# Kernel optimization log

Measured on AMD Instinct MI355X. Metric: run time of the kernel, lower is better.

The kernel has to match this reference:

```python
import jax, jax.numpy as jnp
import numpy as np

NX = 256
NY = 256
H = 1.0          # grid spacing (h == h_sub since scale_sub == 1)
N_ITERS = 512    # parallel (Jacobi) Godunov sweeps; wavefront moves ~1 cell/iter
BIG = 1.0e6      # 'infinity' init for travel times
N_PICKS = 2_000_000


def setup_inputs() -> dict:
    key = jax.random.key(0)
    k1, k2, k3, k4, k5 = jax.random.split(key, 5)
    # slowness f = 1/vp with vp ~ U[5,6] km/s (realistic crustal P velocities)
    vp = 5.0 + jax.random.uniform(k1, (NX, NY), dtype=jnp.float32)
    f = 1.0 / vp
    # station (source) location in grid units, strictly inside the grid
    src_xy = jax.random.uniform(k2, (2,), dtype=jnp.float32) * jnp.array(
        [NX - 1.0, NY - 1.0], dtype=jnp.float32)
    # event locations in grid units and origin times
    event_x = jax.random.uniform(k3, (N_PICKS,), dtype=jnp.float32) * (NX - 1.0)
    event_y = jax.random.uniform(k4, (N_PICKS,), dtype=jnp.float32) * (NY - 1.0)
    event_time = jax.random.normal(k5, (N_PICKS,), dtype=jnp.float32)
    return {"f": f, "src_xy": src_xy, "event_x": event_x,
            "event_y": event_y, "event_time": event_time}


def _st_clamp(x, lo, hi):
    # straight-through clamp (matches torch Clamp.backward: identity grad)
    return x + jax.lax.stop_gradient(jnp.clip(x, lo, hi) - x)


def _eikonal2d(f, src_xy):
    """Godunov upwind eikonal solve |grad u| = f on an NX x NY grid,
    point source at fractional coords src_xy, via fixed-point Jacobi sweeps."""
    sx, sy = src_xy[0], src_xy[1]
    ix0 = jnp.clip(jnp.floor(sx), 0, NX - 2).astype(jnp.int32)
    iy0 = jnp.clip(jnp.floor(sy), 0, NY - 2).astype(jnp.int32)
    # seed the 4 cells around the source with local straight-ray times
    ii = jnp.stack([ix0, ix0, ix0 + 1, ix0 + 1])
    jj = jnp.stack([iy0, iy0 + 1, iy0, iy0 + 1])
    d = jnp.sqrt((ii.astype(f.dtype) - sx) ** 2 +
                 (jj.astype(f.dtype) - sy) ** 2) * H * f[ii, jj]
    u0 = jnp.full((NX, NY), BIG, dtype=f.dtype).at[ii, jj].set(d)
    fh = f * H

    def step(u, _):
        up = jnp.pad(u, 1, constant_values=BIG)
        a = jnp.minimum(up[:-2, 1:-1], up[2:, 1:-1])   # upwind min along x
        b = jnp.minimum(up[1:-1, :-2], up[1:-1, 2:])   # upwind min along y
        one_sided = jnp.minimum(a, b) + fh
        disc = jnp.maximum(2.0 * fh * fh - (a - b) ** 2, 0.0)
        two_sided = 0.5 * (a + b + jnp.sqrt(disc))
        cand = jnp.where(jnp.abs(a - b) >= fh, one_sided, two_sided)
        return jnp.minimum(u, cand), None

    u, _ = jax.lax.scan(step, u0, None, length=N_ITERS)
    return u


def _interp(tt, x, y):
    # bilinear interp exactly as Eikonal2D.interp (floor+clamp, 4 gathers)
    nx, ny = tt.shape
    ix0 = jnp.clip(jnp.floor(x), 0, nx - 2).astype(jnp.int32)
    iy0 = jnp.clip(jnp.floor(y), 0, ny - 2).astype(jnp.int32)
    ix1 = ix0 + 1
    iy1 = iy0 + 1
    xc = _st_clamp(x, 0.0, nx - 1.0)
    yc = _st_clamp(y, 0.0, ny - 1.0)
    Q00 = tt[ix0, iy0]
    Q01 = tt[ix0, iy1]
    Q10 = tt[ix1, iy0]
    Q11 = tt[ix1, iy1]
    return (Q00 * (ix1 - xc) * (iy1 - yc) + Q10 * (xc - ix0) * (iy1 - yc)
            + Q01 * (ix1 - xc) * (yc - iy0) + Q11 * (xc - ix0) * (yc - iy0))


def reference(f, src_xy, event_x, event_y, event_time):
    u = _eikonal2d(f, src_xy)                 # [NX, NY] travel-time table
    tt = _interp(u, event_x, event_y)         # [N] per-pick travel times
    return event_time + tt                    # predicted arrival times [N]
```

## Files before the change

kernel.cpp:

```cpp
#include <hip/hip_runtime.h>
#include <math.h>

#define NXg 256
#define NYg 256
#define BIGV 1.0e6f
#define TB 32
#define KMAX 96
#define NSWEEP 24

__global__ void eik_init(const float* __restrict__ f, const float* __restrict__ src,
                         float* __restrict__ u) {
    int t = blockIdx.x * blockDim.x + threadIdx.x;
    float sx = src[0], sy = src[1];
    int ix0 = (int)fminf(fmaxf(floorf(sx), 0.f), (float)(NXg - 2));
    int iy0 = (int)fminf(fmaxf(floorf(sy), 0.f), (float)(NYg - 2));
#pragma unroll
    for (int k = 0; k < 4; ++k) {
        int cid = t + (k << 14);
        int gx = cid >> 8, gy = cid & 255;
        float val = BIGV;
        if ((gx == ix0 || gx == ix0 + 1) && (gy == iy0 || gy == iy0 + 1)) {
            float dx = (float)gx - sx, dy = (float)gy - sy;
            val = sqrtf(dx * dx + dy * dy) * f[cid];
        }
        u[cid] = val;
    }
}

__global__ __launch_bounds__(256) void eik_sweep(const float* __restrict__ f,
                                                 float* __restrict__ u) {
    __shared__ float us[TB + 2][TB + 2];
    const int t = threadIdx.x;
    const int bx = blockIdx.x & 7, by = blockIdx.x >> 3;
    const int x0 = bx * TB, y0 = by * TB;

    for (int idx = t; idx < (TB + 2) * (TB + 2); idx += 256) {
        int r = idx / (TB + 2), c = idx % (TB + 2);
        int gx = x0 + r - 1, gy = y0 + c - 1;
        float v = BIGV;
        if (gx >= 0 && gx < NXg && gy >= 0 && gy < NYg) v = u[(gx << 8) + gy];
        us[r][c] = v;
    }

    float fhr[4], tfh2[4];
#pragma unroll
    for (int k = 0; k < 4; ++k) {
        int cid = t + (k << 8);
        int r = cid >> 5, c = cid & 31;
        float fv = f[((x0 + r) << 8) + (y0 + c)];
        fhr[k] = fv;
        tfh2[k] = 2.0f * fv * fv;
    }
    __syncthreads();

    for (int it = 0; it < KMAX; ++it) {
        int ch = 0;
#pragma unroll
        for (int k = 0; k < 4; ++k) {
            int cid = t + (k << 8);
            int r = cid >> 5, c = cid & 31;
            float a  = fminf(us[r][c + 1], us[r + 2][c + 1]);
            float b  = fminf(us[r + 1][c], us[r + 1][c + 2]);
            float u0 = us[r + 1][c + 1];
            float one  = fminf(a, b) + fhr[k];
            float diff = a - b;
            float disc = fmaxf(tfh2[k] - diff * diff, 0.f);
            float two  = 0.5f * (a + b + sqrtf(disc));
            float cand = (fabsf(diff) >= fhr[k]) ? one : two;
            if (cand < u0) { us[r + 1][c + 1] = cand; ch = 1; }
        }
        if (__syncthreads_count(ch) == 0) break;
    }

#pragma unroll
    for (int k = 0; k < 4; ++k) {
        int cid = t + (k << 8);
        int r = cid >> 5, c = cid & 31;
        u[((x0 + r) << 8) + (y0 + c)] = us[r + 1][c + 1];
    }
}

__global__ void eik_interp(const float* __restrict__ u,
                           const float* __restrict__ ex,
                           const float* __restrict__ ey,
                           const float* __restrict__ et,
                           float* __restrict__ out, int n) {
    int i = blockIdx.x * blockDim.x + threadIdx.x;
    int stride = gridDim.x * blockDim.x;
    for (; i < n; i += stride) {
        float x = ex[i], y = ey[i];
        int ix0 = (int)fminf(fmaxf(floorf(x), 0.f), (float)(NXg - 2));
        int iy0 = (int)fminf(fmaxf(floorf(y), 0.f), (float)(NYg - 2));
        float xc = fminf(fmaxf(x, 0.f), (float)(NXg - 1));
        float yc = fminf(fmaxf(y, 0.f), (float)(NYg - 1));
        float fx0 = (float)ix0, fy0 = (float)iy0;
        float wx0 = xc - fx0, wx1 = (fx0 + 1.f) - xc;
        float wy0 = yc - fy0, wy1 = (fy0 + 1.f) - yc;
        int base = (ix0 << 8) + iy0;
        float Q00 = u[base],       Q01 = u[base + 1];
        float Q10 = u[base + 256], Q11 = u[base + 257];
        float tt = Q00 * wx1 * wy1 + Q10 * wx0 * wy1
                 + Q01 * wx1 * wy0 + Q11 * wx0 * wy0;
        out[i] = et[i] + tt;
    }
}

extern "C" void kernel_launch(void* const* d_in, const int* in_sizes, int n_in,
                              void* d_out, int out_size, void* d_ws, size_t ws_size,
                              hipStream_t stream) {
    const float* f   = (const float*)d_in[0];
    const float* src = (const float*)d_in[1];
    const float* ex  = (const float*)d_in[2];
    const float* ey  = (const float*)d_in[3];
    const float* et  = (const float*)d_in[4];
    float* out = (float*)d_out;
    float* u   = (float*)d_ws;
    int n = in_sizes[2];

    eik_init<<<64, 256, 0, stream>>>(f, src, u);
    for (int r = 0; r < NSWEEP; ++r)
        eik_sweep<<<64, 256, 0, stream>>>(f, u);
    eik_interp<<<2048, 256, 0, stream>>>(u, ex, ey, et, out, n);
}
```

Baseline: 910.6 us.

## Replace block Jacobi sweeps with wavefront fast-sweeping on 64x64 tiles

Replaces the 32x32-tile Jacobi relaxation with a Gauss-Seidel fast-sweeping scheme on 64x64 tiles. Each wave of 64 threads sweeps the tile along anti-diagonals in one of four directions, using volatile shared memory, and updates values in place. Tiles that hold no finite values exit early. The launch count drops from 24 to 8 rounds of 16 blocks. This should need far fewer iterations to converge, but four waves write the same tile concurrently without synchronisation between diagonal steps, and only 16 blocks occupy the GPU.

```diff
diff --git a/kernel.cpp b/kernel.cpp
--- a/kernel.cpp
+++ b/kernel.cpp
@@ -4,9 +4,10 @@
 #define NXg 256
 #define NYg 256
 #define BIGV 1.0e6f
-#define TB 32
-#define KMAX 96
-#define NSWEEP 24
+#define UP 66
+#define FP 66
+#define NROUNDS 8
+#define MAXSETS 6
 
 __global__ void eik_init(const float* __restrict__ f, const float* __restrict__ src,
                          float* __restrict__ u) {
@@ -27,56 +28,82 @@
     }
 }
 
-__global__ __launch_bounds__(256) void eik_sweep(const float* __restrict__ f,
-                                                 float* __restrict__ u) {
-    __shared__ float us[TB + 2][TB + 2];
+__device__ __forceinline__ float eik_relax(float u0, float a, float b, float fh) {
+    float one  = fminf(a, b) + fh;
+    float diff = a - b;
+    float disc = fmaxf(2.0f * fh * fh - diff * diff, 0.0f);
+    float two  = 0.5f * (a + b + sqrtf(disc));
+    float cand = (fabsf(diff) >= fh) ? one : two;
+    return fminf(u0, cand);
+}
+
+__global__ __launch_bounds__(256) void eik_fsm(const float* __restrict__ f,
+                                               float* __restrict__ u) {
+    __shared__ float uLs[66 * UP];
+    __shared__ float fL[64 * FP];
+    __shared__ int   sflag[4];
+    __shared__ int   s_seen;
+    volatile float* uL = uLs;
+
     const int t = threadIdx.x;
-    const int bx = blockIdx.x & 7, by = blockIdx.x >> 3;
-    const int x0 = bx * TB, y0 = by * TB;
+    const int l = t & 63;
+    const int w = t >> 6;
+    const int bx = blockIdx.x & 3, by = blockIdx.x >> 2;
+    const int x0 = bx * 64, y0 = by * 64;
 
-    for (int idx = t; idx < (TB + 2) * (TB + 2); idx += 256) {
-        int r = idx / (TB + 2), c = idx % (TB + 2);
+    if (t < 4) sflag[t] = 0;
+    if (t == 0) s_seen = 0;
+    __syncthreads();
+
+    int seen = 0;
+    for (int idx = t; idx < 66 * 66; idx += 256) {
+        int r = idx / 66, c = idx % 66;
         int gx = x0 + r - 1, gy = y0 + c - 1;
         float v = BIGV;
         if (gx >= 0 && gx < NXg && gy >= 0 && gy < NYg) v = u[(gx << 8) + gy];
-        us[r][c] = v;
+        uLs[r * UP + c] = v;
+        seen |= (v < BIGV) ? 1 : 0;
+    }
+    for (int idx = t; idx < 64 * 64; idx += 256) {
+        int r = idx >> 6, c = idx & 63;
+        fL[r * FP + c] = f[((x0 + r) << 8) + (y0 + c)];
+    }
+    if (seen) s_seen = 1;
+    __syncthreads();
+    if (!s_seen) return;
+
+    for (int set = 0; set < MAXSETS; ++set) {
+        int changed = 0;
+        for (int tt = 0; tt < 127; ++tt) {
+            int j = (w == 0) ? (tt - l)
+                  : (w == 1) ? (tt - 63 + l)
+                  : (w == 2) ? (63 - tt + l)
+                             : (126 - tt - l);
+            if (j >= 0 && j <= 63) {
+                float u0 = uL[(l + 1) * UP + (j + 1)];
+                float xm = uL[ l      * UP + (j + 1)];
+                float xp = uL[(l + 2) * UP + (j + 1)];
+                float ym = uL[(l + 1) * UP +  j     ];
+                float yp = uL[(l + 1) * UP + (j + 2)];
+                float fh = fL[l * FP + j];
+                float un = eik_relax(u0, fminf(xm, xp), fminf(ym, yp), fh);
+                if (un < u0) { uL[(l + 1) * UP + (j + 1)] = un; changed = 1; }
+            }
+        }
+        int anyc = __any(changed) ? 1 : 0;
+        __syncthreads();
+        if (l == 0) sflag[w] = anyc;
+        __syncthreads();
+        int tot = sflag[0] | sflag[1] | sflag[2] | sflag[3];
+        __syncthreads();
+        if (t < 4) sflag[t] = 0;
+        if (!tot) break;
     }
 
-    float fhr[4], tfh2[4];
-#pragma unroll
-    for (int k = 0; k < 4; ++k) {
-        int cid = t + (k << 8);
-        int r = cid >> 5, c = cid & 31;
-        float fv = f[((x0 + r) << 8) + (y0 + c)];
-        fhr[k] = fv;
-        tfh2[k] = 2.0f * fv * fv;
-    }
     __syncthreads();
-
-    for (int it = 0; it < KMAX; ++it) {
-        int ch = 0;
-#pragma unroll
-        for (int k = 0; k < 4; ++k) {
-            int cid = t + (k << 8);
-            int r = cid >> 5, c = cid & 31;
-            float a  = fminf(us[r][c + 1], us[r + 2][c + 1]);
-            float b  = fminf(us[r + 1][c], us[r + 1][c + 2]);
-            float u0 = us[r + 1][c + 1];
-            float one  = fminf(a, b) + fhr[k];
-            float diff = a - b;
-            float disc = fmaxf(tfh2[k] - diff * diff, 0.f);
-            float two  = 0.5f * (a + b + sqrtf(disc));
-            float cand = (fabsf(diff) >= fhr[k]) ? one : two;
-            if (cand < u0) { us[r + 1][c + 1] = cand; ch = 1; }
-        }
-        if (__syncthreads_count(ch) == 0) break;
-    }
-
-#pragma unroll
-    for (int k = 0; k < 4; ++k) {
-        int cid = t + (k << 8);
-        int r = cid >> 5, c = cid & 31;
-        u[((x0 + r) << 8) + (y0 + c)] = us[r + 1][c + 1];
+    for (int idx = t; idx < 64 * 64; idx += 256) {
+        int r = idx >> 6, c = idx & 63;
+        u[((x0 + r) << 8) + (y0 + c)] = uLs[(r + 1) * UP + (c + 1)];
     }
 }
 
@@ -118,7 +145,7 @@
     int n = in_sizes[2];
 
     eik_init<<<64, 256, 0, stream>>>(f, src, u);
-    for (int r = 0; r < NSWEEP; ++r)
-        eik_sweep<<<64, 256, 0, stream>>>(f, u);
+    for (int r = 0; r < NROUNDS; ++r)
+        eik_fsm<<<16, 256, 0, stream>>>(f, u);
     eik_interp<<<2048, 256, 0, stream>>>(u, ex, ey, et, out, n);
 }
```

Result: slower. 1.831 ms (+101.0%).

## Solve eikonal in one block with fast-sweeping wavefronts over fp16 shared grid

Applied to the files above, without the earlier changes.

Replaces the 24 launches of tiled Jacobi sweeps with a single-block solver. The whole 256x256 travel-time grid is held in LDS as fp16 values rounded upward. Each of the four wavefronts runs a Gauss-Seidel fast sweep from a different corner as an anti-diagonal wavefront across lanes, passing neighbour values by shuffles and repeating until nothing changes. The aim is to cut the launch count and the many Jacobi iterations, but everything now runs on one CU and the fp16 storage loses precision in the travel times.

```diff
diff --git a/kernel.cpp b/kernel.cpp
--- a/kernel.cpp
+++ b/kernel.cpp
@@ -1,83 +1,115 @@
 #include <hip/hip_runtime.h>
+#include <hip/hip_fp16.h>
 #include <math.h>
 
-#define NXg 256
-#define NYg 256
-#define BIGV 1.0e6f
-#define TB 32
-#define KMAX 96
-#define NSWEEP 24
+#define BIGF   57344.0f
+#define BIG2   0x7B007B00u
+#define MAXSETS 8
 
-__global__ void eik_init(const float* __restrict__ f, const float* __restrict__ src,
-                         float* __restrict__ u) {
-    int t = blockIdx.x * blockDim.x + threadIdx.x;
-    float sx = src[0], sy = src[1];
-    int ix0 = (int)fminf(fmaxf(floorf(sx), 0.f), (float)(NXg - 2));
-    int iy0 = (int)fminf(fmaxf(floorf(sy), 0.f), (float)(NYg - 2));
-#pragma unroll
-    for (int k = 0; k < 4; ++k) {
-        int cid = t + (k << 14);
-        int gx = cid >> 8, gy = cid & 255;
-        float val = BIGV;
-        if ((gx == ix0 || gx == ix0 + 1) && (gy == iy0 || gy == iy0 + 1)) {
-            float dx = (float)gx - sx, dy = (float)gy - sy;
-            val = sqrtf(dx * dx + dy * dy) * f[cid];
-        }
-        u[cid] = val;
-    }
+
+__device__ __forceinline__ float relax1(float u0, float a, float b, float fh) {
+    float one  = fminf(a, b) + fh;
+    float diff = a - b;
+    float disc = fmaxf(2.0f * fh * fh - diff * diff, 0.0f);
+    float two  = 0.5f * (a + b + sqrtf(disc));
+    float cand = (fabsf(diff) >= fh) ? one : two;
+    return fminf(u0, cand);
 }
 
-__global__ __launch_bounds__(256) void eik_sweep(const float* __restrict__ f,
-                                                 float* __restrict__ u) {
-    __shared__ float us[TB + 2][TB + 2];
-    const int t = threadIdx.x;
-    const int bx = blockIdx.x & 7, by = blockIdx.x >> 3;
-    const int x0 = bx * TB, y0 = by * TB;
+__device__ __forceinline__ unsigned short f2h_up(float x) {
+    __half h = __float2half(x);
+    if (__half2float(h) < x)
+        h = __ushort_as_half((unsigned short)(__half_as_ushort(h) + 1));
+    return __half_as_ushort(h);
+}
 
-    for (int idx = t; idx < (TB + 2) * (TB + 2); idx += 256) {
-        int r = idx / (TB + 2), c = idx % (TB + 2);
-        int gx = x0 + r - 1, gy = y0 + c - 1;
-        float v = BIGV;
-        if (gx >= 0 && gx < NXg && gy >= 0 && gy < NYg) v = u[(gx << 8) + gy];
-        us[r][c] = v;
+__global__ __launch_bounds__(256) void eik_solve(const float* __restrict__ f,
+                                                 const float* __restrict__ src,
+                                                 float* __restrict__ u_out) {
+    __shared__ unsigned short uW[65536];
+    const int t = threadIdx.x, l = t & 63, w = t >> 6;
+
+    {
+        unsigned int* p = (unsigned int*)uW;
+        for (int i = t; i < 32768; i += 256) p[i] = BIG2;
     }
-
-    float fhr[4], tfh2[4];
-#pragma unroll
-    for (int k = 0; k < 4; ++k) {
-        int cid = t + (k << 8);
-        int r = cid >> 5, c = cid & 31;
-        float fv = f[((x0 + r) << 8) + (y0 + c)];
-        fhr[k] = fv;
-        tfh2[k] = 2.0f * fv * fv;
+    __syncthreads();
+    if (t < 4) {
+        float sx = src[0], sy = src[1];
+        int ix0 = (int)fminf(fmaxf(floorf(sx), 0.f), 254.f);
+        int iy0 = (int)fminf(fmaxf(floorf(sy), 0.f), 254.f);
+        int gx = ix0 + (t >> 1), gy = iy0 + (t & 1);
+        float dx = (float)gx - sx, dy = (float)gy - sy;
+        float v = sqrtf(dx * dx + dy * dy) * f[(gx << 8) + gy];
+        uW[(gx << 8) + gy] = f2h_up(v);
     }
     __syncthreads();
 
-    for (int it = 0; it < KMAX; ++it) {
-        int ch = 0;
-#pragma unroll
-        for (int k = 0; k < 4; ++k) {
-            int cid = t + (k << 8);
-            int r = cid >> 5, c = cid & 31;
-            float a  = fminf(us[r][c + 1], us[r + 2][c + 1]);
-            float b  = fminf(us[r + 1][c], us[r + 1][c + 2]);
-            float u0 = us[r + 1][c + 1];
-            float one  = fminf(a, b) + fhr[k];
-            float diff = a - b;
-            float disc = fmaxf(tfh2[k] - diff * diff, 0.f);
-            float two  = 0.5f * (a + b + sqrtf(disc));
-            float cand = (fabsf(diff) >= fhr[k]) ? one : two;
-            if (cand < u0) { us[r + 1][c + 1] = cand; ch = 1; }
-        }
-        if (__syncthreads_count(ch) == 0) break;
+    const int xflip = w & 1, yflip = (w >> 1) & 1;
+    const int C0 = l << 2;
+    const int xk0 = xflip ? 255 - C0 : C0;
+    const int dxk = xflip ? -1 : 1;
+    const int ub0 = (xk0) << 8,            ub1 = (xk0 + dxk) << 8;
+    const int ub2 = (xk0 + 2 * dxk) << 8,  ub3 = (xk0 + 3 * dxk) << 8;
+    const float* fB0 = f + ub0; const float* fB1 = f + ub1;
+    const float* fB2 = f + ub2; const float* fB3 = f + ub3;
+
+#define YPHYS(S, K) ({ int yl_ = (S) - C0 - (K);                                \
+                       int yc_ = min(max(yl_, 0), 255);                         \
+                       yflip ? 255 - yc_ : yc_; })
+
+#define KSTEP(K, XM, YM, UN) {                                                  \
+        const int Y  = Yb - (K);                                                \
+        const int ycp = yflip ? 255 - min(max(Y, 0), 255)                       \
+                              : min(max(Y, 0), 255);                            \
+        const int off = ub##K + ycp;                                            \
+        unsigned short ob = uW[off];                                            \
+        float u0 = __half2float(__ushort_as_half(ob));                          \
+        float nu = relax1(u0, (XM), (YM), fr##K[i]);                            \
+        if (Y >= 0 && Y <= 255) {                                               \
+            unsigned short nb = f2h_up(nu);                                     \
+            if (nb < ob) { uW[off] = nb; changed = 1; }                         \
+            UN = nu;                                                            \
+        }                                                                       \
     }
 
+    for (int set = 0; set < MAXSETS; ++set) {
+        int changed = 0;
+        float un0 = BIGF, un1 = BIGF, un2 = BIGF, un3 = BIGF;
+        float fr0[8], fr1[8], fr2[8], fr3[8];
 #pragma unroll
-    for (int k = 0; k < 4; ++k) {
-        int cid = t + (k << 8);
-        int r = cid >> 5, c = cid & 31;
-        u[((x0 + r) << 8) + (y0 + c)] = us[r + 1][c + 1];
+        for (int i = 0; i < 8; ++i) {
+            fr0[i] = fB0[YPHYS(i, 0)];
+            fr1[i] = fB1[YPHYS(i, 1)];
+            fr2[i] = fB2[YPHYS(i, 2)];
+            fr3[i] = fB3[YPHYS(i, 3)];
+        }
+        for (int sb = 0; sb < 512; sb += 8) {
+#pragma unroll
+            for (int i = 0; i < 8; ++i) {
+                const int s_ = sb + i;
+                const int Yb = s_ - C0;
+                float o0 = un0, o1 = un1, o2 = un2, o3 = un3;
+                float sh = __shfl_up(un3, 1, 64);
+                if (l == 0) sh = BIGF;
+                KSTEP(0, sh, o0, un0)
+                KSTEP(1, o0, o1, un1)
+                KSTEP(2, o1, o2, un2)
+                KSTEP(3, o2, o3, un3)
+                fr0[i] = fB0[YPHYS(s_ + 8, 0)];
+                fr1[i] = fB1[YPHYS(s_ + 8, 1)];
+                fr2[i] = fB2[YPHYS(s_ + 8, 2)];
+                fr3[i] = fB3[YPHYS(s_ + 8, 3)];
+            }
+        }
+        if (__syncthreads_count(changed) == 0) break;
     }
+    __syncthreads();
+
+    for (int idx = t; idx < 65536; idx += 256)
+        u_out[idx] = __half2float(__ushort_as_half(uW[idx]));
+#undef KSTEP
+#undef YPHYS
 }
 
 __global__ void eik_interp(const float* __restrict__ u,
@@ -89,10 +121,10 @@
     int stride = gridDim.x * blockDim.x;
     for (; i < n; i += stride) {
         float x = ex[i], y = ey[i];
-        int ix0 = (int)fminf(fmaxf(floorf(x), 0.f), (float)(NXg - 2));
-        int iy0 = (int)fminf(fmaxf(floorf(y), 0.f), (float)(NYg - 2));
-        float xc = fminf(fmaxf(x, 0.f), (float)(NXg - 1));
-        float yc = fminf(fmaxf(y, 0.f), (float)(NYg - 1));
+        int ix0 = (int)fminf(fmaxf(floorf(x), 0.f), 254.f);
+        int iy0 = (int)fminf(fmaxf(floorf(y), 0.f), 254.f);
+        float xc = fminf(fmaxf(x, 0.f), 255.f);
+        float yc = fminf(fmaxf(y, 0.f), 255.f);
         float fx0 = (float)ix0, fy0 = (float)iy0;
         float wx0 = xc - fx0, wx1 = (fx0 + 1.f) - xc;
         float wy0 = yc - fy0, wy1 = (fy0 + 1.f) - yc;
@@ -113,12 +145,10 @@
     const float* ex  = (const float*)d_in[2];
     const float* ey  = (const float*)d_in[3];
     const float* et  = (const float*)d_in[4];
-    float* out = (float*)d_out;
-    float* u   = (float*)d_ws;
+    float* out   = (float*)d_out;
+    float* u_out = (float*)d_ws;
     int n = in_sizes[2];
 
-    eik_init<<<64, 256, 0, stream>>>(f, src, u);
-    for (int r = 0; r < NSWEEP; ++r)
-        eik_sweep<<<64, 256, 0, stream>>>(f, u);
-    eik_interp<<<2048, 256, 0, stream>>>(u, ex, ey, et, out, n);
+    eik_solve<<<1, 256, 0, stream>>>(f, src, u_out);
+    eik_interp<<<2048, 256, 0, stream>>>(u_out, ex, ey, et, out, n);
 }
```

After: 2.038 ms. 124% more time.
